# Optimization experiments

Measured on AMD Instinct MI355X. Metric: run time of the kernel, lower is better.

## Reference

```python
import jax, jax.numpy as jnp
import numpy as np

D_MODEL = 1024
N_HEADS = 16
D_HEAD = D_MODEL // N_HEADS


def setup_inputs() -> dict:
    key = jax.random.key(0)
    k1, k2, k3, k4, k5 = jax.random.split(key, 5)
    B, S = 2, 2048
    scale_in = 1.0 / np.sqrt(D_MODEL)
    return {
        "x": jax.random.normal(k1, (B, S, D_MODEL), dtype=jnp.float32),
        "qkv_w": jax.random.normal(k2, (3 * D_MODEL, D_MODEL), dtype=jnp.float32) * scale_in,
        "qkv_b": jax.random.normal(k3, (3 * D_MODEL,), dtype=jnp.float32) * 0.02,
        "out_w": jax.random.normal(k4, (D_MODEL, D_MODEL), dtype=jnp.float32) * scale_in,
        "out_b": jax.random.normal(k5, (D_MODEL,), dtype=jnp.float32) * 0.02,
    }


def reference(x, qkv_w, qkv_b, out_w, out_b) -> jnp.ndarray:
    B, S, D = x.shape
    # qkv projection: torch Linear stores weight as (out, in)
    qkv = x @ qkv_w.T + qkv_b                      # [B,S,3D]
    qkv = qkv.reshape(B, S, 3, N_HEADS, D_HEAD)
    qkv = jnp.transpose(qkv, (2, 0, 3, 1, 4))      # [3,B,H,S,d]
    q, k, v = qkv[0], qkv[1], qkv[2]
    scale = 1.0 / np.sqrt(D_HEAD).astype(np.float32)
    scores = jnp.einsum("bhsd,bhtd->bhst", q, k) * scale  # [B,H,S,S]
    attn = jax.nn.softmax(scores, axis=-1)
    out = jnp.einsum("bhst,bhtd->bhsd", attn, v)   # [B,H,S,d]
    out = jnp.transpose(out, (0, 2, 1, 3)).reshape(B, S, D)
    return out @ out_w.T + out_b
```

## Files before the change

### kernel.cpp

```cpp
#include <hip/hip_runtime.h>

typedef __bf16 bf16;
typedef __bf16 bf16x4 __attribute__((ext_vector_type(4)));
typedef __bf16 bf16x8 __attribute__((ext_vector_type(8)));
typedef float  f32x4  __attribute__((ext_vector_type(4)));

__device__ __forceinline__ void gld16(const void* g, void* l) {
  __builtin_amdgcn_global_load_lds(
      (const __attribute__((address_space(1))) void*)g,
      (__attribute__((address_space(3))) void*)l, 16, 0, 0);
}

__global__ void f2bf_all(const float* __restrict__ x, bf16* __restrict__ xo,
                         const float* __restrict__ w1, bf16* __restrict__ w1o,
                         const float* __restrict__ w2, bf16* __restrict__ w2o) {
  int i = blockIdx.x * blockDim.x + threadIdx.x;
  const float* in; bf16* out; int idx;
  if (i < 1048576)      { in = x;  out = xo;  idx = i; }
  else if (i < 1835008) { in = w1; out = w1o; idx = i - 1048576; }
  else                  { in = w2; out = w2o; idx = i - 1835008; }
  float4 v = reinterpret_cast<const float4*>(in)[idx];
  bf16x4 o = { (bf16)v.x, (bf16)v.y, (bf16)v.z, (bf16)v.w };
  reinterpret_cast<bf16x4*>(out)[idx] = o;
}

template<int MODE, int BN>
__global__ __launch_bounds__(256)
void gemm_bt(const bf16* __restrict__ A, const bf16* __restrict__ B,
             const float* __restrict__ bias, void* __restrict__ Cout,
             int K, int N) {
  __shared__ bf16 As[128 * 64];
  __shared__ bf16 Bs[BN * 64];
  const int tid  = threadIdx.x;
  const int wave = tid >> 6, lane = tid & 63;
  const int quad = lane >> 4, l16 = lane & 15;
  const int bm = blockIdx.x * 128, bn = blockIdx.y * BN;
  constexpr int NI  = (BN == 128) ? 4 : 2;
  constexpr int BCH = BN / 32;
  const int wr = (BN == 128) ? (wave >> 1) * 64 : wave * 32;
  const int wc = (BN == 128) ? (wave & 1) * 64 : 0;
  const int arow = lane >> 3;
  const int acol = (lane & 7) * 8;

  f32x4 acc[NI][4] = {};

  const bf16* Ab = A + (size_t)bm * K;
  const bf16* Bb = B + (size_t)bn * K;

  for (int k0 = 0; k0 < K; k0 += 64) {
#pragma unroll
    for (int i = 0; i < 4; ++i) {
      int c = wave * 4 + i;
      gld16(Ab + (size_t)(c * 8 + arow) * K + k0 + acol, As + c * 512);
    }
#pragma unroll
    for (int i = 0; i < BCH; ++i) {
      int c = wave * BCH + i;
      gld16(Bb + (size_t)(c * 8 + arow) * K + k0 + acol, Bs + c * 512);
    }
    __syncthreads();
#pragma unroll
    for (int kk = 0; kk < 64; kk += 32) {
      bf16x8 af[NI], bfr[4];
#pragma unroll
      for (int i = 0; i < NI; ++i)
        af[i]  = *(const bf16x8*)(As + (wr + i * 16 + l16) * 64 + kk + quad * 8);
#pragma unroll
      for (int j = 0; j < 4; ++j)
        bfr[j] = *(const bf16x8*)(Bs + (wc + j * 16 + l16) * 64 + kk + quad * 8);
#pragma unroll
      for (int i = 0; i < NI; ++i)
#pragma unroll
        for (int j = 0; j < 4; ++j)
          acc[i][j] = __builtin_amdgcn_mfma_f32_16x16x32_bf16(af[i], bfr[j], acc[i][j], 0, 0, 0);
    }
    __syncthreads();
  }

  if constexpr (MODE == 0) {
    bf16* Q = (bf16*)Cout;
#pragma unroll
    for (int j = 0; j < 4; ++j) {
      int col = bn + wc + j * 16 + l16;
      float bv  = bias[col];
      int sec = col >> 10, rem = col & 1023;
      int h = rem >> 6, d = rem & 63;
      if (sec < 2) {
        float scl = (sec == 0) ? 0.125f * 1.44269504f : 1.0f;
#pragma unroll
        for (int i = 0; i < NI; ++i) {
#pragma unroll
          for (int r = 0; r < 4; ++r) {
            int row = bm + wr + i * 16 + quad * 4 + r;
            int b = row >> 11, si = row & 2047;
            float v = (acc[i][j][r] + bv) * scl;
            Q[(((size_t)sec * 32 + b * 16 + h) * 2048 + si) * 64 + d] = (bf16)v;
          }
        }
      } else {
#pragma unroll
        for (int i = 0; i < NI; ++i) {
          int row0 = bm + wr + i * 16 + quad * 4;
          int b = row0 >> 11, si = row0 & 2047;
          bf16x4 pk = { (bf16)(acc[i][j][0] + bv), (bf16)(acc[i][j][1] + bv),
                        (bf16)(acc[i][j][2] + bv), (bf16)(acc[i][j][3] + bv) };
          *(bf16x4*)(Q + (size_t)2 * 4194304 +
                     ((size_t)(b * 16 + h) * 64 + d) * 2048 + si) = pk;
        }
      }
    }
  } else {
    float* C = (float*)Cout;
#pragma unroll
    for (int j = 0; j < 4; ++j) {
      int col = bn + wc + j * 16 + l16;
      float bv = bias[col];
#pragma unroll
      for (int i = 0; i < NI; ++i)
#pragma unroll
        for (int r = 0; r < 4; ++r) {
          int row = bm + wr + i * 16 + quad * 4 + r;
          C[(size_t)row * N + col] = acc[i][j][r] + bv;
        }
    }
  }
}

__global__ __launch_bounds__(256, 2)
void attn_kernel(const bf16* __restrict__ QKV, const bf16* __restrict__ Vt,
                 bf16* __restrict__ O) {
  __shared__ bf16 Ks[2][128 * 72];
  __shared__ bf16 Ps[4][32 * 136];

  const int bh = blockIdx.x;
  const int q0 = blockIdx.y * 128;
  const bf16* Qg = QKV + ((size_t)bh * 2048 + q0) * 64;
  const bf16* Kg = QKV + (size_t)32 * 2048 * 64 + (size_t)bh * 2048 * 64;
  const bf16* Vg = Vt + (size_t)bh * 64 * 2048;

  const int tid  = threadIdx.x;
  const int wave = tid >> 6, lane = tid & 63;
  const int quad = lane >> 4, l16 = lane & 15;
  const int srow = tid >> 3;
  const int scol = (tid & 7) * 8;
  bf16* Pw = &Ps[wave][0];

  bf16x8 aq[2][2];
#pragma unroll
  for (int i = 0; i < 2; ++i)
#pragma unroll
    for (int kh = 0; kh < 2; ++kh)
      aq[i][kh] = *(const bf16x8*)(Qg + (size_t)(wave * 32 + i * 16 + l16) * 64 +
                                   kh * 32 + quad * 8);

  {
    bf16x8 kreg[4];
#pragma unroll
    for (int ch = 0; ch < 4; ++ch)
      kreg[ch] = *(const bf16x8*)(Kg + (size_t)(ch * 32 + srow) * 64 + scol);
#pragma unroll
    for (int ch = 0; ch < 4; ++ch)
      *(bf16x8*)(&Ks[0][(ch * 32 + srow) * 72 + scol]) = kreg[ch];
  }
  __syncthreads();

  float rs[2] = {0.f, 0.f};
  f32x4 o[2][4] = {};

  for (int kt = 0; kt < 16; ++kt) {
    const int cur = kt & 1;

    bf16x8 kreg[4];
    if (kt < 15) {
#pragma unroll
      for (int ch = 0; ch < 4; ++ch)
        kreg[ch] = *(const bf16x8*)(Kg + (size_t)((kt + 1) * 128 + ch * 32 + srow) * 64 + scol);
    }
    bf16x8 bv[4][4];
#pragma unroll
    for (int kk = 0; kk < 4; ++kk)
#pragma unroll
      for (int oj = 0; oj < 4; ++oj)
        bv[kk][oj] = *(const bf16x8*)(Vg + (size_t)(oj * 16 + l16) * 2048 +
                                      kt * 128 + kk * 32 + quad * 8);

    f32x4 s[2][8] = {};
#pragma unroll
    for (int kh = 0; kh < 2; ++kh) {
#pragma unroll
      for (int ni = 0; ni < 8; ++ni) {
        bf16x8 bk = *(const bf16x8*)(&Ks[cur][(ni * 16 + l16) * 72 + kh * 32 + quad * 8]);
        s[0][ni] = __builtin_amdgcn_mfma_f32_16x16x32_bf16(bk, aq[0][kh], s[0][ni], 0, 0, 0);
        s[1][ni] = __builtin_amdgcn_mfma_f32_16x16x32_bf16(bk, aq[1][kh], s[1][ni], 0, 0, 0);
      }
    }

    if (kt < 15) {
#pragma unroll
      for (int ch = 0; ch < 4; ++ch)
        *(bf16x8*)(&Ks[cur ^ 1][(ch * 32 + srow) * 72 + scol]) = kreg[ch];
    }

#pragma unroll
    for (int i = 0; i < 2; ++i)
#pragma unroll
      for (int ni = 0; ni < 8; ++ni) {
        float p0 = __builtin_amdgcn_exp2f(s[i][ni][0]);
        float p1 = __builtin_amdgcn_exp2f(s[i][ni][1]);
        float p2 = __builtin_amdgcn_exp2f(s[i][ni][2]);
        float p3 = __builtin_amdgcn_exp2f(s[i][ni][3]);
        rs[i] += (p0 + p1) + (p2 + p3);
        bf16x4 pk = { (bf16)p0, (bf16)p1, (bf16)p2, (bf16)p3 };
        *(bf16x4*)(Pw + (i * 16 + l16) * 136 + ni * 16 + quad * 4) = pk;
      }

#pragma unroll
    for (int kk = 0; kk < 4; ++kk) {
#pragma unroll
      for (int i = 0; i < 2; ++i) {
        bf16x8 ap = *(const bf16x8*)(Pw + (i * 16 + l16) * 136 + kk * 32 + quad * 8);
#pragma unroll
        for (int oj = 0; oj < 4; ++oj)
          o[i][oj] = __builtin_amdgcn_mfma_f32_16x16x32_bf16(ap, bv[kk][oj], o[i][oj], 0, 0, 0);
      }
    }

    __syncthreads();
  }

#pragma unroll
  for (int i = 0; i < 2; ++i) {
    rs[i] += __shfl_xor(rs[i], 16);
    rs[i] += __shfl_xor(rs[i], 32);
  }

  const int b = bh >> 4, h = bh & 15;
#pragma unroll
  for (int i = 0; i < 2; ++i)
#pragma unroll
    for (int r = 0; r < 4; ++r) {
      float lsum = __shfl(rs[i], quad * 4 + r);
      float inv = 1.0f / lsum;
      int row = q0 + wave * 32 + i * 16 + quad * 4 + r;
#pragma unroll
      for (int oj = 0; oj < 4; ++oj)
        O[((size_t)(b * 2048 + row)) * 1024 + h * 64 + oj * 16 + l16] =
            (bf16)(o[i][oj][r] * inv);
    }
}

extern "C" void kernel_launch(void* const* d_in, const int* in_sizes, int n_in,
                              void* d_out, int out_size, void* d_ws, size_t ws_size,
                              hipStream_t stream) {
  const float* x      = (const float*)d_in[0];
  const float* qkv_w  = (const float*)d_in[1];
  const float* qkv_b  = (const float*)d_in[2];
  const float* out_w  = (const float*)d_in[3];
  const float* out_b  = (const float*)d_in[4];
  float* out = (float*)d_out;

  char* ws = (char*)d_ws;
  bf16* Xb   = (bf16*)(ws);
  bf16* Wqkv = (bf16*)(ws + 8388608);
  bf16* Wout = (bf16*)(ws + 14680064);
  bf16* QKV  = (bf16*)(ws + 16777216);
  bf16* At   = (bf16*)(ws + 41943040);
  bf16* VtP  = QKV + (size_t)2 * 32 * 2048 * 64;

  f2bf_all<<<8192, 256, 0, stream>>>(x, Xb, qkv_w, Wqkv, out_w, Wout);

  gemm_bt<0, 128><<<dim3(32, 24), 256, 0, stream>>>(Xb, Wqkv, qkv_b, (void*)QKV, 1024, 3072);

  attn_kernel<<<dim3(32, 16), 256, 0, stream>>>(QKV, VtP, At);

  gemm_bt<1, 64><<<dim3(32, 16), 256, 0, stream>>>(At, Wout, out_b, (void*)out, 1024, 1024);
}
```

Baseline: 224.3 us.

## Shrink attention tiles to 64 queries and 64-key blocks for higher occupancy

The attention kernel now gives each wave 16 query rows instead of 32, and each block 64 queries instead of 128. Keys stream in 64-row tiles over 32 iterations. The grid doubles to 1024 blocks and launch bounds allow 4 blocks per CU, so occupancy and latency hiding should improve on the large CU count. In exchange, K and V are reloaded twice as often per query, and there are more barriers and less MFMA reuse per loaded K/V fragment.

```diff
diff --git a/kernel.cpp b/kernel.cpp
--- a/kernel.cpp
+++ b/kernel.cpp
@@ -126,14 +126,14 @@
   }
 }
 
-__global__ __launch_bounds__(256, 2)
+__global__ __launch_bounds__(256, 4)
 void attn_kernel(const bf16* __restrict__ QKV, const bf16* __restrict__ Vt,
                  bf16* __restrict__ O) {
-  __shared__ bf16 Ks[2][128 * 72];
-  __shared__ bf16 Ps[4][32 * 136];
+  __shared__ bf16 Ks[2][64 * 72];
+  __shared__ bf16 Ps[4][16 * 136];
 
   const int bh = blockIdx.x;
-  const int q0 = blockIdx.y * 128;
+  const int q0 = blockIdx.y * 64;
   const bf16* Qg = QKV + ((size_t)bh * 2048 + q0) * 64;
   const bf16* Kg = QKV + (size_t)32 * 2048 * 64 + (size_t)bh * 2048 * 64;
   const bf16* Vg = Vt + (size_t)bh * 64 * 2048;
@@ -145,108 +145,95 @@
   const int scol = (tid & 7) * 8;
   bf16* Pw = &Ps[wave][0];
 
-  bf16x8 aq[2][2];
-#pragma unroll
-  for (int i = 0; i < 2; ++i)
-#pragma unroll
-    for (int kh = 0; kh < 2; ++kh)
-      aq[i][kh] = *(const bf16x8*)(Qg + (size_t)(wave * 32 + i * 16 + l16) * 64 +
-                                   kh * 32 + quad * 8);
+  bf16x8 aq[2];
+#pragma unroll
+  for (int kh = 0; kh < 2; ++kh)
+    aq[kh] = *(const bf16x8*)(Qg + (size_t)(wave * 16 + l16) * 64 +
+                              kh * 32 + quad * 8);
 
   {
-    bf16x8 kreg[4];
-#pragma unroll
-    for (int ch = 0; ch < 4; ++ch)
+    bf16x8 kreg[2];
+#pragma unroll
+    for (int ch = 0; ch < 2; ++ch)
       kreg[ch] = *(const bf16x8*)(Kg + (size_t)(ch * 32 + srow) * 64 + scol);
 #pragma unroll
-    for (int ch = 0; ch < 4; ++ch)
+    for (int ch = 0; ch < 2; ++ch)
       *(bf16x8*)(&Ks[0][(ch * 32 + srow) * 72 + scol]) = kreg[ch];
   }
   __syncthreads();
 
-  float rs[2] = {0.f, 0.f};
-  f32x4 o[2][4] = {};
-
-  for (int kt = 0; kt < 16; ++kt) {
+  float rs = 0.f;
+  f32x4 o[4] = {};
+
+  for (int kt = 0; kt < 32; ++kt) {
     const int cur = kt & 1;
 
-    bf16x8 kreg[4];
-    if (kt < 15) {
-#pragma unroll
-      for (int ch = 0; ch < 4; ++ch)
-        kreg[ch] = *(const bf16x8*)(Kg + (size_t)((kt + 1) * 128 + ch * 32 + srow) * 64 + scol);
-    }
-    bf16x8 bv[4][4];
-#pragma unroll
-    for (int kk = 0; kk < 4; ++kk)
+    bf16x8 kreg[2];
+    if (kt < 31) {
+#pragma unroll
+      for (int ch = 0; ch < 2; ++ch)
+        kreg[ch] = *(const bf16x8*)(Kg + (size_t)((kt + 1) * 64 + ch * 32 + srow) * 64 + scol);
+    }
+    bf16x8 bv[2][4];
+#pragma unroll
+    for (int kk = 0; kk < 2; ++kk)
 #pragma unroll
       for (int oj = 0; oj < 4; ++oj)
         bv[kk][oj] = *(const bf16x8*)(Vg + (size_t)(oj * 16 + l16) * 2048 +
-                                      kt * 128 + kk * 32 + quad * 8);
-
-    f32x4 s[2][8] = {};
+                                      kt * 64 + kk * 32 + quad * 8);
+
+    f32x4 s[4] = {};
 #pragma unroll
     for (int kh = 0; kh < 2; ++kh) {
 #pragma unroll
-      for (int ni = 0; ni < 8; ++ni) {
+      for (int ni = 0; ni < 4; ++ni) {
         bf16x8 bk = *(const bf16x8*)(&Ks[cur][(ni * 16 + l16) * 72 + kh * 32 + quad * 8]);
-        s[0][ni] = __builtin_amdgcn_mfma_f32_16x16x32_bf16(bk, aq[0][kh], s[0][ni], 0, 0, 0);
-        s[1][ni] = __builtin_amdgcn_mfma_f32_16x16x32_bf16(bk, aq[1][kh], s[1][ni], 0, 0, 0);
+        s[ni] = __builtin_amdgcn_mfma_f32_16x16x32_bf16(bk, aq[kh], s[ni], 0, 0, 0);
       }
     }
 
-    if (kt < 15) {
-#pragma unroll
-      for (int ch = 0; ch < 4; ++ch)
+    if (kt < 31) {
+#pragma unroll
+      for (int ch = 0; ch < 2; ++ch)
         *(bf16x8*)(&Ks[cur ^ 1][(ch * 32 + srow) * 72 + scol]) = kreg[ch];
     }
 
 #pragma unroll
-    for (int i = 0; i < 2; ++i)
-#pragma unroll
-      for (int ni = 0; ni < 8; ++ni) {
-        float p0 = __builtin_amdgcn_exp2f(s[i][ni][0]);
-        float p1 = __builtin_amdgcn_exp2f(s[i][ni][1]);
-        float p2 = __builtin_amdgcn_exp2f(s[i][ni][2]);
-        float p3 = __builtin_amdgcn_exp2f(s[i][ni][3]);
-        rs[i] += (p0 + p1) + (p2 + p3);
-        bf16x4 pk = { (bf16)p0, (bf16)p1, (bf16)p2, (bf16)p3 };
-        *(bf16x4*)(Pw + (i * 16 + l16) * 136 + ni * 16 + quad * 4) = pk;
-      }
-
-#pragma unroll
-    for (int kk = 0; kk < 4; ++kk) {
-#pragma unroll
-      for (int i = 0; i < 2; ++i) {
-        bf16x8 ap = *(const bf16x8*)(Pw + (i * 16 + l16) * 136 + kk * 32 + quad * 8);
-#pragma unroll
-        for (int oj = 0; oj < 4; ++oj)
-          o[i][oj] = __builtin_amdgcn_mfma_f32_16x16x32_bf16(ap, bv[kk][oj], o[i][oj], 0, 0, 0);
-      }
+    for (int ni = 0; ni < 4; ++ni) {
+      float p0 = __builtin_amdgcn_exp2f(s[ni][0]);
+      float p1 = __builtin_amdgcn_exp2f(s[ni][1]);
+      float p2 = __builtin_amdgcn_exp2f(s[ni][2]);
+      float p3 = __builtin_amdgcn_exp2f(s[ni][3]);
+      rs += (p0 + p1) + (p2 + p3);
+      bf16x4 pk = { (bf16)p0, (bf16)p1, (bf16)p2, (bf16)p3 };
+      *(bf16x4*)(Pw + l16 * 136 + ni * 16 + quad * 4) = pk;
+    }
+
+#pragma unroll
+    for (int kk = 0; kk < 2; ++kk) {
+      bf16x8 ap = *(const bf16x8*)(Pw + l16 * 136 + kk * 32 + quad * 8);
+#pragma unroll
+      for (int oj = 0; oj < 4; ++oj)
+        o[oj] = __builtin_amdgcn_mfma_f32_16x16x32_bf16(ap, bv[kk][oj], o[oj], 0, 0, 0);
     }
 
     __syncthreads();
   }
 
-#pragma unroll
-  for (int i = 0; i < 2; ++i) {
-    rs[i] += __shfl_xor(rs[i], 16);
-    rs[i] += __shfl_xor(rs[i], 32);
-  }
+  rs += __shfl_xor(rs, 16);
+  rs += __shfl_xor(rs, 32);
 
   const int b = bh >> 4, h = bh & 15;
 #pragma unroll
-  for (int i = 0; i < 2; ++i)
-#pragma unroll
-    for (int r = 0; r < 4; ++r) {
-      float lsum = __shfl(rs[i], quad * 4 + r);
-      float inv = 1.0f / lsum;
-      int row = q0 + wave * 32 + i * 16 + quad * 4 + r;
-#pragma unroll
-      for (int oj = 0; oj < 4; ++oj)
-        O[((size_t)(b * 2048 + row)) * 1024 + h * 64 + oj * 16 + l16] =
-            (bf16)(o[i][oj][r] * inv);
-    }
+  for (int r = 0; r < 4; ++r) {
+    float lsum = __shfl(rs, quad * 4 + r);
+    float inv = 1.0f / lsum;
+    int row = q0 + wave * 16 + quad * 4 + r;
+#pragma unroll
+    for (int oj = 0; oj < 4; ++oj)
+      O[((size_t)(b * 2048 + row)) * 1024 + h * 64 + oj * 16 + l16] =
+          (bf16)(o[oj][r] * inv);
+  }
 }
 
 extern "C" void kernel_launch(void* const* d_in, const int* in_sizes, int n_in,
@@ -271,7 +258,7 @@
 
   gemm_bt<0, 128><<<dim3(32, 24), 256, 0, stream>>>(Xb, Wqkv, qkv_b, (void*)QKV, 1024, 3072);
 
-  attn_kernel<<<dim3(32, 16), 256, 0, stream>>>(QKV, VtP, At);
+  attn_kernel<<<dim3(32, 32), 256, 0, stream>>>(QKV, VtP, At);
 
   gemm_bt<1, 64><<<dim3(32, 16), 256, 0, stream>>>(At, Wout, out_b, (void*)out, 1024, 1024);
 }
```

Result: slower. 280.8 us (+25.2%).
